# Performance work log

Measured on AMD Instinct MI355X. Metric: run time of the kernel, lower is better.

Reference implementation:

```python
import jax, jax.numpy as jnp
import numpy as np

L = 14  # max_relative_position
H = 12  # num_heads
HD = 64  # head_dim


def rel_pos_embed(N, table_v, table_h):
    # 2D relative-position embedding with a leading CLS token (index 0).
    n = N - 1
    s = int(n ** 0.5)  # grid side (14)
    r = jnp.arange(n)
    dv = r[None, :] // s - r[:, None] // s  # vertical distance
    dh = r[None, :] % s - r[:, None] % s   # horizontal distance
    iv = jnp.clip(dv, -L, L) + L + 1
    ih = jnp.clip(dh, -L, L) + L + 1
    iv = jnp.pad(iv, ((1, 0), (1, 0)))  # CLS row/col -> index 0
    ih = jnp.pad(ih, ((1, 0), (1, 0)))
    return table_v[iv] + table_h[ih]  # [N, N, HD]


def setup_inputs() -> dict:
    key = jax.random.key(0)
    ks = jax.random.split(key, 11)
    B, N, E = 64, 197, 768
    T = 2 * L + 2  # rel-pos table rows (30)
    std = 0.02
    return {
        "x": jax.random.normal(ks[0], (B, N, E), jnp.float32),
        "wq": jax.random.normal(ks[1], (E, H * HD), jnp.float32) * std,
        "wk": jax.random.normal(ks[2], (E, H * HD), jnp.float32) * std,
        "wv": jax.random.normal(ks[3], (E, H * HD), jnp.float32) * std,
        "wproj": jax.random.normal(ks[4], (H * HD, E), jnp.float32) * std,
        "bproj": jnp.zeros((E,), jnp.float32),
        "rk_v": jax.random.normal(ks[5], (T, HD), jnp.float32) * std,
        "rk_h": jax.random.normal(ks[6], (T, HD), jnp.float32) * std,
        "rv_v": jax.random.normal(ks[7], (T, HD), jnp.float32) * std,
        "rv_h": jax.random.normal(ks[8], (T, HD), jnp.float32) * std,
    }


def reference(x, wq, wk, wv, wproj, bproj, rk_v, rk_h, rv_v, rv_h):
    B, N, E = x.shape
    scale = HD ** -0.5
    q = (x @ wq).reshape(B, N, H, HD).transpose(0, 2, 1, 3)  # [B,H,N,HD]
    k = (x @ wk).reshape(B, N, H, HD).transpose(0, 2, 1, 3)
    v = (x @ wv).reshape(B, N, H, HD).transpose(0, 2, 1, 3)

    attn = jnp.einsum('bhid,bhjd->bhij', q, k) * scale
    rpk = rel_pos_embed(N, rk_v, rk_h)  # [N,N,HD]
    attn = attn + jnp.einsum('bhid,ijd->bhij', q, rpk) * scale
    attn = jax.nn.softmax(attn, axis=-1)

    out = jnp.einsum('bhij,bhjd->bhid', attn, v)
    rpv = rel_pos_embed(N, rv_v, rv_h)
    out = out + jnp.einsum('bhij,ijd->bhid', attn, rpv)

    out = out.transpose(0, 2, 1, 3).reshape(B, N, H * HD)
    return out @ wproj + bproj
```

## Files before the change

### kernel.cpp

```cpp
#include <hip/hip_runtime.h>
#include <math.h>

typedef _Float16 f16;
typedef __attribute__((ext_vector_type(8))) _Float16 f16x8;
typedef __attribute__((ext_vector_type(4))) _Float16 f16x4;
typedef __attribute__((ext_vector_type(4))) float f32x4;

#define NH 12
#define HDIM 64
#define NTOK 197
#define EDIM 768
#define NB 64
#define MROWS (NB*NTOK)

__device__ __forceinline__ void wfence() {
    asm volatile("s_waitcnt lgkmcnt(0)" ::: "memory");
    __builtin_amdgcn_sched_barrier(0);
    __builtin_amdgcn_wave_barrier();
}

__device__ __forceinline__ unsigned div14(unsigned n) { return (n * 4682u) >> 16; }

__device__ __forceinline__ void gload16(const f16* g, f16* lds_base) {
    __builtin_amdgcn_global_load_lds(
        (const __attribute__((address_space(1))) void*)g,
        (__attribute__((address_space(3))) void*)lds_base, 16, 0, 0);
}

__global__ __launch_bounds__(256) void prep_all(
    const float* __restrict__ x,
    const float* __restrict__ wq, const float* __restrict__ wk,
    const float* __restrict__ wv, const float* __restrict__ wp,
    const float* __restrict__ rkv, const float* __restrict__ rkh,
    f16* __restrict__ xh, f16* __restrict__ wqkvT, f16* __restrict__ wpT,
    f16* __restrict__ gA, f16* __restrict__ gt_buf)
{
    __shared__ float T[64][65];
    const int bid = blockIdx.x;
    if (bid < 4728) {
        int idx = bid * 256 + threadIdx.x;
        const float4* s = (const float4*)x + (size_t)idx * 2;
        float4 a = s[0], b = s[1];
        f16x8 h;
        h[0]=(f16)a.x; h[1]=(f16)a.y; h[2]=(f16)a.z; h[3]=(f16)a.w;
        h[4]=(f16)b.x; h[5]=(f16)b.y; h[6]=(f16)b.z; h[7]=(f16)b.w;
        *(f16x8*)(xh + (size_t)idx * 8) = h;
    } else if (bid < 5304) {
        int b2 = bid - 4728;
        int m = b2 / 144, rem = b2 - m*144;
        const float* src = (m==0)?wq:(m==1)?wk:(m==2)?wv:wp;
        int k0 = (rem / 12) * 64, n0 = (rem % 12) * 64;
        int cidx = threadIdx.x & 63, r4 = threadIdx.x >> 6;
#pragma unroll
        for (int rr = 0; rr < 16; ++rr) {
            int kl = rr*4 + r4;
            T[kl][cidx] = src[(size_t)(k0+kl)*EDIM + n0 + cidx];
        }
        __syncthreads();
        f16* dst = (m < 3) ? (wqkvT + (size_t)m*EDIM*EDIM) : wpT;
#pragma unroll
        for (int rr = 0; rr < 16; ++rr) {
            int nl = rr*4 + r4;
            dst[(size_t)(n0+nl)*EDIM + k0 + cidx] = (f16)T[cidx][nl];
        }
    } else {
        int t = (bid - 5304) * 256 + threadIdx.x;
        const int stride = 32 * 256;
        for (int i = t; i < 272*128; i += stride) {
            int row = i >> 7, cs = i & 127;
            int c = cs ^ ((row & 7) << 3);
            f16 v = (f16)0.f;
            if (c < 64) {
                if (row >= 208 && row < 238)      v = (f16)rkv[(row-208)*64 + c];
                else if (row >= 240 && row < 270) v = (f16)rkh[(row-240)*64 + c];
            } else if (c < 96 && row < 208) {
                int g = c - 64;
                if (row == 0) { if (g == 14 || g == 30) v = (f16)1.f; }
                else if (row <= 196) {
                    int rm = row - 1;
                    int gv = (int)div14((unsigned)rm), gh = rm - gv*14;
                    if (g == gv || g == 16 + gh) v = (f16)1.f;
                }
            }
            gA[i] = v;
        }
        for (int i = t; i < 32*256; i += stride) {
            int g = i >> 8, cs = i & 255;
            int j = cs ^ ((g & 7) << 3);
            f16 v = (f16)0.f;
            if (j >= 1 && j <= 196) {
                int jm = j - 1;
                int gv = (int)div14((unsigned)jm), gh = jm - gv*14;
                if ((g < 14 && gv == g) || (g >= 16 && g < 30 && gh == g - 16))
                    v = (f16)1.f;
            }
            gt_buf[i] = v;
        }
    }
}

__global__ __launch_bounds__(512, 2) void gemm256(
    const f16* __restrict__ A, const f16* __restrict__ Bt,
    f16* __restrict__ q_o, f16* __restrict__ k_o, f16* __restrict__ v_o,
    float* __restrict__ p_o, const float* __restrict__ bias, int mode, int nxb)
{
    __shared__ f16 lds[4*16384];

    const int tid = threadIdx.x;
    const int l = tid & 63, w = tid >> 6;
    const int lr = l & 15, lq = l >> 4;
    const int wr = w >> 2, wc = w & 3;

    const int nwg = gridDim.x, orig = blockIdx.x;
    const int xcd = orig & 7, qc = nwg >> 3, rc = nwg & 7;
    const int wgid = (xcd < rc ? xcd*(qc+1) : rc*(qc+1) + (xcd-rc)*qc) + (orig >> 3);
    const int mband = wgid / nxb, nband = wgid - mband*nxb;
    const int m0 = mband << 8, n0 = nband << 8;

    const int scol = (((tid & 7) ^ ((tid >> 3) & 7)) << 3);
    const f16* aG[4]; const f16* bG[4];
#pragma unroll
    for (int p = 0; p < 4; ++p) {
        int rt = p*64 + (tid >> 3);
        int ra = m0 + rt; if (ra >= MROWS) ra = MROWS - 1;
        aG[p] = A  + (size_t)ra * EDIM + scol;
        bG[p] = Bt + (size_t)(n0 + rt) * EDIM + scol;
    }
    const int lbase = w * 512;

    f32x4 acc[8][4];
#pragma unroll
    for (int mt = 0; mt < 8; ++mt)
#pragma unroll
        for (int nt = 0; nt < 4; ++nt) {
            acc[mt][nt][0]=0.f; acc[mt][nt][1]=0.f;
            acc[mt][nt][2]=0.f; acc[mt][nt][3]=0.f;
        }

#pragma unroll
    for (int p = 0; p < 4; ++p) {
        gload16(aG[p], &lds[p*4096 + lbase]);
        gload16(bG[p], &lds[32768 + p*4096 + lbase]);
    }
    asm volatile("s_waitcnt vmcnt(0)" ::: "memory");
    __builtin_amdgcn_sched_barrier(0);
    __builtin_amdgcn_s_barrier();

    const int swz = (lr & 7) << 3;
    int cur = 0;
    for (int kt = 0; kt < 12; ++kt) {
        if (kt < 11) {
            const int ko = (kt + 1) * 64;
            const int nb = (cur ^ 1) * 16384;
#pragma unroll
            for (int p = 0; p < 4; ++p) {
                gload16(aG[p] + ko, &lds[nb + p*4096 + lbase]);
                gload16(bG[p] + ko, &lds[32768 + nb + p*4096 + lbase]);
            }
        }
        __builtin_amdgcn_sched_barrier(0);
        const f16* Ab = &lds[cur * 16384];
        const f16* Bb = &lds[32768 + cur * 16384];
#pragma unroll
        for (int ks = 0; ks < 2; ++ks) {
            const int kb = (ks*32 + lq*8) ^ swz;
            f16x8 bf[4];
#pragma unroll
            for (int nt = 0; nt < 4; ++nt)
                bf[nt] = *(const f16x8*)&Bb[(wc*64 + nt*16 + lr)*64 + kb];
#pragma unroll
            for (int mt = 0; mt < 8; ++mt) {
                f16x8 af = *(const f16x8*)&Ab[(wr*128 + mt*16 + lr)*64 + kb];
#pragma unroll
                for (int nt = 0; nt < 4; ++nt)
                    acc[mt][nt] = __builtin_amdgcn_mfma_f32_16x16x32_f16(
                        af, bf[nt], acc[mt][nt], 0, 0, 0);
            }
        }
        asm volatile("s_waitcnt vmcnt(0)" ::: "memory");
        __builtin_amdgcn_sched_barrier(0);
        __builtin_amdgcn_s_barrier();
        cur ^= 1;
    }

    if (mode == 0) {
        const int mat   = n0 / EDIM;
        const int hbase = ((n0 % EDIM) >> 6) + wc;
        f16* dst = (mat == 0) ? q_o : (mat == 1) ? k_o : v_o;
        f16* scr = &lds[w * 2304];
#pragma unroll
        for (int mt2 = 0; mt2 < 4; ++mt2) {
#pragma unroll
            for (int mtp = 0; mtp < 2; ++mtp) {
                const int mt = mt2*2 + mtp;
#pragma unroll
                for (int nt = 0; nt < 4; ++nt)
#pragma unroll
                    for (int rg = 0; rg < 4; ++rg)
                        scr[(mtp*16 + lq*4 + rg)*72 + nt*16 + lr] = (f16)acc[mt][nt][rg];
            }
            wfence();
#pragma unroll
            for (int i = 0; i < 4; ++i) {
                int row = (l >> 3) + i*8;
                f16x8 v = *(const f16x8*)&scr[row*72 + (l & 7)*8];
                int R = m0 + wr*128 + mt2*32 + row;
                if (R < MROWS) {
                    int bb = R / NTOK, nn = R - bb*NTOK;
                    *(f16x8*)&dst[((size_t)(bb*NH + hbase)*NTOK + nn)*HDIM + (l & 7)*8] = v;
                }
            }
            wfence();
        }
    } else {
#pragma unroll
        for (int mt = 0; mt < 8; ++mt)
#pragma unroll
            for (int rg = 0; rg < 4; ++rg) {
                int R = m0 + wr*128 + mt*16 + lq*4 + rg;
                if (R < MROWS) {
                    float* base = p_o + (size_t)R * EDIM + n0 + wc*64;
#pragma unroll
                    for (int nt = 0; nt < 4; ++nt) {
                        int c = nt*16 + lr;
                        base[c] = acc[mt][nt][rg] + bias[n0 + wc*64 + c];
                    }
                }
            }
    }
}

#define SKE 128
#define SVT 320
#define SGT 256
#define SWS 72
#define ATHR 832

__global__ __launch_bounds__(ATHR, 1) void attn_mfma(
    const f16* __restrict__ q_ws, const f16* __restrict__ k_ws,
    const f16* __restrict__ v_ws,
    const float* __restrict__ rvv, const float* __restrict__ rvh,
    const f16* __restrict__ gA, const f16* __restrict__ gt_buf,
    f16* __restrict__ o_ws)
{
    __shared__ f16 Kle[272*SKE];
    __shared__ f16 Vt[64*SVT];
    __shared__ f16 Gt[32*SGT];
    __shared__ f16 WSh[13*16*SWS];

    const int tid = threadIdx.x;
    const int w = tid >> 6, l = tid & 63;
    const int lr = l & 15, lq = l >> 4;
    const int bh = blockIdx.x;
    const int b = bh / NH, h = bh - b * NH;
    const f16* Qp = q_ws + (size_t)bh * NTOK * HDIM;
    const f16* Kp = k_ws + (size_t)bh * NTOK * HDIM;
    const f16* Vp = v_ws + (size_t)bh * NTOK * HDIM;
    f16* wsh = &WSh[w * 16 * SWS];

    for (int idx = tid; idx < 272*16; idx += ATHR) {
        int row = idx >> 4, cs8 = (idx & 15) << 3;
        f16x8 v;
        if (row < NTOK && cs8 < 64) {
            int c8 = cs8 ^ ((row & 7) << 3);
            v = *(const f16x8*)(Kp + row*64 + c8);
        } else {
            v = *(const f16x8*)(gA + row*SKE + cs8);
        }
        *(f16x8*)&Kle[row*SKE + cs8] = v;
    }
    for (int idx = tid; idx < 32*32; idx += ATHR) {
        int off = idx * 8;
        *(f16x8*)&Gt[off] = *(const f16x8*)(gt_buf + off);
    }
    for (int idx = tid; idx < 8*SVT; idx += ATHR) {
        int dlow = idx & 7, k = idx >> 3;
        int kx = k ^ (dlow << 3);
        bool isV = (k < NTOK), isA = (k >= 208 && k < 238), isB = (k >= 238 && k < 268);
#pragma unroll
        for (int e = 0; e < 8; ++e) {
            int d = (e << 3) + dlow;
            f16 val = (f16)0.f;
            if (isV)      val = Vp[k*64 + d];
            else if (isA) val = (f16)rvv[(k-208)*64 + d];
            else if (isB) val = (f16)rvh[(k-238)*64 + d];
            Vt[d*SVT + kx] = val;
        }
    }
    __syncthreads();

    const int src0 = ((l >> 4) & 1) * 32 + lr;
    const int src1 = src0 + 16;

    {
        const int tt = w;
        const int i0 = tt * 16;
        const int iq = i0 + lr;
        const int iqc = (iq > 196) ? 196 : iq;
        const f16* qsrc = Qp + iqc*64 + lq*8;
        f16x8 qf0 = *(const f16x8*)qsrc;
        f16x8 qf1 = *(const f16x8*)(qsrc + 32);

        const int sw = (lr & 7) << 3;

        __builtin_amdgcn_s_setprio(1);
        f32x4 pacc[4];
#pragma unroll
        for (int ct = 0; ct < 4; ++ct) {
            f32x4 a; a[0]=0.f; a[1]=0.f; a[2]=0.f; a[3]=0.f;
            const int krow = (13+ct)*16 + lr;
            f16x8 kf0 = *(f16x8*)&Kle[krow*SKE + ((lq*8) ^ sw)];
            f16x8 kf1 = *(f16x8*)&Kle[krow*SKE + ((32 + lq*8) ^ sw)];
            a = __builtin_amdgcn_mfma_f32_16x16x32_f16(kf0, qf0, a, 0, 0, 0);
            a = __builtin_amdgcn_mfma_f32_16x16x32_f16(kf1, qf1, a, 0, 0, 0);
            pacc[ct] = a;
        }
        __builtin_amdgcn_s_setprio(0);
#pragma unroll
        for (int ct = 0; ct < 4; ++ct)
#pragma unroll
            for (int rg = 0; rg < 4; ++rg)
                wsh[lr*SWS + ct*16 + lq*4 + rg] = (f16)pacc[ct][rg];
        wfence();

        int id_ = 0, ih_ = 0;
        const bool qcls = (iq == 0);
        if (iq > 0) { unsigned v = div14((unsigned)(iq-1)); id_ = (int)v; ih_ = (iq-1) - (int)v*14; }
        f16x8 qcf;
#pragma unroll
        for (int e = 0; e < 8; ++e) {
            int g = lq*8 + e;
            int toff;
            if (g < 14)       toff = qcls ? 0 : (g - id_ + 15);
            else if (g == 14) toff = 0;
            else if (g == 15) toff = 63;
            else if (g < 30)  toff = qcls ? 32 : (32 + (g-16) - ih_ + 15);
            else if (g == 30) toff = 32;
            else              toff = 63;
            qcf[e] = wsh[lr*SWS + toff];
        }

        f32x4 acc[13];
        __builtin_amdgcn_s_setprio(1);
#pragma unroll
        for (int ct = 0; ct < 13; ++ct) {
            f32x4 a; a[0]=0.f; a[1]=0.f; a[2]=0.f; a[3]=0.f;
            const int krow = ct*16 + lr;
            f16x8 kf0 = *(f16x8*)&Kle[krow*SKE + ((lq*8) ^ sw)];
            f16x8 kf1 = *(f16x8*)&Kle[krow*SKE + ((32 + lq*8) ^ sw)];
            f16x8 gf  = *(f16x8*)&Kle[krow*SKE + ((64 + lq*8) ^ sw)];
            a = __builtin_amdgcn_mfma_f32_16x16x32_f16(kf0, qf0, a, 0, 0, 0);
            a = __builtin_amdgcn_mfma_f32_16x16x32_f16(kf1, qf1, a, 0, 0, 0);
            a = __builtin_amdgcn_mfma_f32_16x16x32_f16(gf,  qcf, a, 0, 0, 0);
            acc[ct] = a;
        }
        __builtin_amdgcn_s_setprio(0);

#pragma unroll
        for (int rg = 0; rg < 4; ++rg)
            if (lq*4 + rg > 4) acc[12][rg] = -1e30f;

        float m = -1e30f;
#pragma unroll
        for (int ct = 0; ct < 13; ++ct)
#pragma unroll
            for (int rg = 0; rg < 4; ++rg) m = fmaxf(m, acc[ct][rg]);
        m = fmaxf(m, __shfl_xor(m, 16));
        m = fmaxf(m, __shfl_xor(m, 32));
        const float C1 = 0.125f * 1.44269504088896f;
        const float nm = -m * C1;
        float ssum = 0.f;
#pragma unroll
        for (int ct = 0; ct < 13; ++ct)
#pragma unroll
            for (int rg = 0; rg < 4; ++rg) {
                float p = exp2f(fmaf(acc[ct][rg], C1, nm));
                acc[ct][rg] = p; ssum += p;
            }
        ssum += __shfl_xor(ssum, 16);
        ssum += __shfl_xor(ssum, 32);
        const float inv = 1.f / ssum;
        const float pn00 = acc[0][0] * inv;

        unsigned pk[13][2];
#pragma unroll
        for (int ct = 0; ct < 13; ++ct) {
            union { f16x4 hh; unsigned u[2]; } t;
            t.hh[0] = (f16)(acc[ct][0] * inv);
            t.hh[1] = (f16)(acc[ct][1] * inv);
            t.hh[2] = (f16)(acc[ct][2] * inv);
            t.hh[3] = (f16)(acc[ct][3] * inv);
            pk[ct][0] = t.u[0]; pk[ct][1] = t.u[1];
        }

        f16x8 pa[7];
#pragma unroll
        for (int kc = 0; kc < 7; ++kc) {
            const int ctA = 2*kc;
            const int ctB = (kc == 6) ? 12 : 2*kc + 1;
            unsigned A0 = (unsigned)__shfl((int)pk[ctA][0], src0);
            unsigned A1 = (unsigned)__shfl((int)pk[ctA][1], src0);
            unsigned A2 = (unsigned)__shfl((int)pk[ctA][0], src1);
            unsigned A3 = (unsigned)__shfl((int)pk[ctA][1], src1);
            unsigned B0 = (unsigned)__shfl((int)pk[ctB][0], src0);
            unsigned B1 = (unsigned)__shfl((int)pk[ctB][1], src0);
            unsigned B2 = (unsigned)__shfl((int)pk[ctB][0], src1);
            unsigned B3 = (unsigned)__shfl((int)pk[ctB][1], src1);
            bool hiHalf = (lq >= 2);
            union { unsigned u[4]; f16x8 v; } f;
            f.u[0] = hiHalf ? B0 : A0;
            f.u[1] = hiHalf ? B1 : A1;
            f.u[2] = hiHalf ? B2 : A2;
            f.u[3] = hiHalf ? B3 : A3;
            if (kc == 6 && hiHalf) { f.u[0]=0; f.u[1]=0; f.u[2]=0; f.u[3]=0; }
            pa[kc] = f.v;
        }

        f32x4 gacc[2];
#pragma unroll
        for (int ct = 0; ct < 2; ++ct) { gacc[ct][0]=0.f; gacc[ct][1]=0.f; gacc[ct][2]=0.f; gacc[ct][3]=0.f; }
        __builtin_amdgcn_s_setprio(1);
#pragma unroll
        for (int kc = 0; kc < 7; ++kc) {
#pragma unroll
            for (int ct = 0; ct < 2; ++ct) {
                f16x8 gf = *(f16x8*)&Gt[(ct*16 + lr)*SGT + ((kc*32 + lq*8) ^ sw)];
                gacc[ct] = __builtin_amdgcn_mfma_f32_16x16x32_f16(pa[kc], gf, gacc[ct], 0, 0, 0);
            }
        }
        __builtin_amdgcn_s_setprio(0);

#pragma unroll
        for (int z = 0; z < 2; ++z) {
            int zi = z*64 + l;
            int zr = zi >> 3, zc = (zi & 7) << 3;
            f16x8 zz;
#pragma unroll
            for (int e = 0; e < 8; ++e) zz[e] = (f16)0.f;
            *(f16x8*)&wsh[zr*SWS + zc] = zz;
        }
        wfence();
#pragma unroll
        for (int rg = 0; rg < 4; ++rg) {
            int il = lq*4 + rg;
            int is_ = i0 + il;
            if (lr < 14 && is_ > 0) {
                unsigned v = div14((unsigned)(is_-1));
                int id2 = (int)v, ih2 = (is_-1) - (int)v*14;
                wsh[il*SWS + (lr - id2 + 15)]      = (f16)gacc[0][rg];
                wsh[il*SWS + 30 + (lr - ih2 + 15)] = (f16)gacc[1][rg];
            }
        }
        if (lq == 0 && !(i0 == 0 && lr == 0)) {
            wsh[lr*SWS + 0]  = (f16)pn00;
            wsh[lr*SWS + 30] = (f16)pn00;
        }
        if (i0 == 0) {
            float sv = (lq == 0) ? gacc[0][0] : 0.f;
            float sh = (lq == 0) ? gacc[1][0] : 0.f;
            sv += __shfl_xor(sv, 1); sv += __shfl_xor(sv, 2);
            sv += __shfl_xor(sv, 4); sv += __shfl_xor(sv, 8);
            sh += __shfl_xor(sh, 1); sh += __shfl_xor(sh, 2);
            sh += __shfl_xor(sh, 4); sh += __shfl_xor(sh, 8);
            if (l == 0) {
                wsh[0]  = (f16)(sv + pn00);
                wsh[30] = (f16)(sh + pn00);
            }
        }
        wfence();

        f16x8 sfr[2];
#pragma unroll
        for (int kc2 = 0; kc2 < 2; ++kc2)
            sfr[kc2] = *(f16x8*)&wsh[lr*SWS + kc2*32 + lq*8];

        f32x4 oacc[4];
#pragma unroll
        for (int ct = 0; ct < 4; ++ct) { oacc[ct][0]=0.f; oacc[ct][1]=0.f; oacc[ct][2]=0.f; oacc[ct][3]=0.f; }
        __builtin_amdgcn_s_setprio(1);
#pragma unroll
        for (int kc = 0; kc < 7; ++kc) {
#pragma unroll
            for (int ct = 0; ct < 4; ++ct) {
                f16x8 vf = *(f16x8*)&Vt[(ct*16 + lr)*SVT + ((kc*32 + lq*8) ^ sw)];
                oacc[ct] = __builtin_amdgcn_mfma_f32_16x16x32_f16(pa[kc], vf, oacc[ct], 0, 0, 0);
            }
        }
#pragma unroll
        for (int kc2 = 0; kc2 < 2; ++kc2) {
#pragma unroll
            for (int ct = 0; ct < 4; ++ct) {
                f16x8 vf = *(f16x8*)&Vt[(ct*16 + lr)*SVT + ((208 + kc2*32 + lq*8) ^ sw)];
                oacc[ct] = __builtin_amdgcn_mfma_f32_16x16x32_f16(sfr[kc2], vf, oacc[ct], 0, 0, 0);
            }
        }
        __builtin_amdgcn_s_setprio(0);

#pragma unroll
        for (int ct = 0; ct < 4; ++ct)
#pragma unroll
            for (int rg = 0; rg < 4; ++rg) {
                int io = i0 + lq*4 + rg;
                if (io < NTOK) {
                    int d = ct*16 + lr;
                    o_ws[((size_t)(b * NTOK + io) * NH + h) * HDIM + d] = (f16)oacc[ct][rg];
                }
            }
    }
}

extern "C" void kernel_launch(void* const* d_in, const int* in_sizes, int n_in,
                              void* d_out, int out_size, void* d_ws, size_t ws_size,
                              hipStream_t stream)
{
    const float* x     = (const float*)d_in[0];
    const float* wq    = (const float*)d_in[1];
    const float* wk    = (const float*)d_in[2];
    const float* wv    = (const float*)d_in[3];
    const float* wproj = (const float*)d_in[4];
    const float* bproj = (const float*)d_in[5];
    const float* rkv   = (const float*)d_in[6];
    const float* rkh   = (const float*)d_in[7];
    const float* rvv   = (const float*)d_in[8];
    const float* rvh   = (const float*)d_in[9];

    f16* ws = (f16*)d_ws;
    const size_t sz = (size_t)MROWS * EDIM;
    f16* xh    = ws;
    f16* qh    = xh + sz;
    f16* kh    = qh + sz;
    f16* vh    = kh + sz;
    f16* oh    = vh + sz;
    f16* wqkvT = oh + sz;
    f16* wpT   = wqkvT + (size_t)3*EDIM*EDIM;
    f16* gA    = wpT   + (size_t)EDIM*EDIM;
    f16* gtb   = gA    + 272*128;

    prep_all<<<5336, 256, 0, stream>>>(x, wq, wk, wv, wproj, rkv, rkh,
                                       xh, wqkvT, wpT, gA, gtb);
    gemm256 <<<50*9, 512, 0, stream>>>(xh, wqkvT, qh, kh, vh,
                                       nullptr, nullptr, 0, 9);
    attn_mfma<<<NB * NH, ATHR, 0, stream>>>(qh, kh, vh,
                                            rvv, rvh, gA, gtb, oh);
    gemm256 <<<50*3, 512, 0, stream>>>(oh, wpT, nullptr, nullptr, nullptr,
                                       (float*)d_out, bproj, 1, 3);
}
```

Measured before the change: 148.1 us.

## Fuse x fp32-to-fp16 conversion into QKV GEMM and async-load attention K/G tiles

After: 150.5 us. Within noise of the previous version (+1.6%).

```diff
diff --git a/kernel.cpp b/kernel.cpp
--- a/kernel.cpp
+++ b/kernel.cpp
@@ -28,26 +28,16 @@
 }
 
 __global__ __launch_bounds__(256) void prep_all(
-    const float* __restrict__ x,
     const float* __restrict__ wq, const float* __restrict__ wk,
     const float* __restrict__ wv, const float* __restrict__ wp,
     const float* __restrict__ rkv, const float* __restrict__ rkh,
-    f16* __restrict__ xh, f16* __restrict__ wqkvT, f16* __restrict__ wpT,
+    f16* __restrict__ wqkvT, f16* __restrict__ wpT,
     f16* __restrict__ gA, f16* __restrict__ gt_buf)
 {
     __shared__ float T[64][65];
     const int bid = blockIdx.x;
-    if (bid < 4728) {
-        int idx = bid * 256 + threadIdx.x;
-        const float4* s = (const float4*)x + (size_t)idx * 2;
-        float4 a = s[0], b = s[1];
-        f16x8 h;
-        h[0]=(f16)a.x; h[1]=(f16)a.y; h[2]=(f16)a.z; h[3]=(f16)a.w;
-        h[4]=(f16)b.x; h[5]=(f16)b.y; h[6]=(f16)b.z; h[7]=(f16)b.w;
-        *(f16x8*)(xh + (size_t)idx * 8) = h;
-    } else if (bid < 5304) {
-        int b2 = bid - 4728;
-        int m = b2 / 144, rem = b2 - m*144;
+    if (bid < 576) {
+        int m = bid / 144, rem = bid - m*144;
         const float* src = (m==0)?wq:(m==1)?wk:(m==2)?wv:wp;
         int k0 = (rem / 12) * 64, n0 = (rem % 12) * 64;
         int cidx = threadIdx.x & 63, r4 = threadIdx.x >> 6;
@@ -64,7 +54,7 @@
             dst[(size_t)(n0+nl)*EDIM + k0 + cidx] = (f16)T[cidx][nl];
         }
     } else {
-        int t = (bid - 5304) * 256 + threadIdx.x;
+        int t = (bid - 576) * 256 + threadIdx.x;
         const int stride = 32 * 256;
         for (int i = t; i < 272*128; i += stride) {
             int row = i >> 7, cs = i & 127;
@@ -99,8 +89,9 @@
     }
 }
 
-__global__ __launch_bounds__(512, 2) void gemm256(
-    const f16* __restrict__ A, const f16* __restrict__ Bt,
+template<bool AF32>
+__global__ __launch_bounds__(512, 2) void gemm256T(
+    const void* __restrict__ Ain, const f16* __restrict__ Bt,
     f16* __restrict__ q_o, f16* __restrict__ k_o, f16* __restrict__ v_o,
     float* __restrict__ p_o, const float* __restrict__ bias, int mode, int nxb)
 {
@@ -118,15 +109,19 @@
     const int m0 = mband << 8, n0 = nband << 8;
 
     const int scol = (((tid & 7) ^ ((tid >> 3) & 7)) << 3);
-    const f16* aG[4]; const f16* bG[4];
+    const f16* bG[4];
+    const f16* aGh[4];
+    const float* aGf[4];
 #pragma unroll
     for (int p = 0; p < 4; ++p) {
         int rt = p*64 + (tid >> 3);
         int ra = m0 + rt; if (ra >= MROWS) ra = MROWS - 1;
-        aG[p] = A  + (size_t)ra * EDIM + scol;
+        if (AF32) aGf[p] = (const float*)Ain + (size_t)ra * EDIM + ((tid & 7) << 3);
+        else      aGh[p] = (const f16*)Ain + (size_t)ra * EDIM + scol;
         bG[p] = Bt + (size_t)(n0 + rt) * EDIM + scol;
     }
     const int lbase = w * 512;
+    const int dstA = (tid >> 3)*64 + scol;
 
     f32x4 acc[8][4];
 #pragma unroll
@@ -137,14 +132,32 @@
             acc[mt][nt][2]=0.f; acc[mt][nt][3]=0.f;
         }
 
-#pragma unroll
-    for (int p = 0; p < 4; ++p) {
-        gload16(aG[p], &lds[p*4096 + lbase]);
+    float4 ar0[4], ar1[4];
+#pragma unroll
+    for (int p = 0; p < 4; ++p)
         gload16(bG[p], &lds[32768 + p*4096 + lbase]);
-    }
-    asm volatile("s_waitcnt vmcnt(0)" ::: "memory");
-    __builtin_amdgcn_sched_barrier(0);
-    __builtin_amdgcn_s_barrier();
+    if (AF32) {
+#pragma unroll
+        for (int p = 0; p < 4; ++p) {
+            ar0[p] = *(const float4*)(aGf[p]);
+            ar1[p] = *(const float4*)(aGf[p] + 4);
+        }
+#pragma unroll
+        for (int p = 0; p < 4; ++p) {
+            f16x8 h;
+            h[0]=(f16)ar0[p].x; h[1]=(f16)ar0[p].y; h[2]=(f16)ar0[p].z; h[3]=(f16)ar0[p].w;
+            h[4]=(f16)ar1[p].x; h[5]=(f16)ar1[p].y; h[6]=(f16)ar1[p].z; h[7]=(f16)ar1[p].w;
+            *(f16x8*)&lds[p*4096 + dstA] = h;
+        }
+        __syncthreads();
+    } else {
+#pragma unroll
+        for (int p = 0; p < 4; ++p)
+            gload16(aGh[p], &lds[p*4096 + lbase]);
+        asm volatile("s_waitcnt vmcnt(0)" ::: "memory");
+        __builtin_amdgcn_sched_barrier(0);
+        __builtin_amdgcn_s_barrier();
+    }
 
     const int swz = (lr & 7) << 3;
     int cur = 0;
@@ -153,9 +166,18 @@
             const int ko = (kt + 1) * 64;
             const int nb = (cur ^ 1) * 16384;
 #pragma unroll
-            for (int p = 0; p < 4; ++p) {
-                gload16(aG[p] + ko, &lds[nb + p*4096 + lbase]);
+            for (int p = 0; p < 4; ++p)
                 gload16(bG[p] + ko, &lds[32768 + nb + p*4096 + lbase]);
+            if (AF32) {
+#pragma unroll
+                for (int p = 0; p < 4; ++p) {
+                    ar0[p] = *(const float4*)(aGf[p] + ko);
+                    ar1[p] = *(const float4*)(aGf[p] + ko + 4);
+                }
+            } else {
+#pragma unroll
+                for (int p = 0; p < 4; ++p)
+                    gload16(aGh[p] + ko, &lds[nb + p*4096 + lbase]);
             }
         }
         __builtin_amdgcn_sched_barrier(0);
@@ -177,9 +199,23 @@
                         af, bf[nt], acc[mt][nt], 0, 0, 0);
             }
         }
-        asm volatile("s_waitcnt vmcnt(0)" ::: "memory");
-        __builtin_amdgcn_sched_barrier(0);
-        __builtin_amdgcn_s_barrier();
+        if (AF32) {
+            if (kt < 11) {
+                const int nb = (cur ^ 1) * 16384;
+#pragma unroll
+                for (int p = 0; p < 4; ++p) {
+                    f16x8 h;
+                    h[0]=(f16)ar0[p].x; h[1]=(f16)ar0[p].y; h[2]=(f16)ar0[p].z; h[3]=(f16)ar0[p].w;
+                    h[4]=(f16)ar1[p].x; h[5]=(f16)ar1[p].y; h[6]=(f16)ar1[p].z; h[7]=(f16)ar1[p].w;
+                    *(f16x8*)&lds[nb + p*4096 + dstA] = h;
+                }
+            }
+            __syncthreads();
+        } else {
+            asm volatile("s_waitcnt vmcnt(0)" ::: "memory");
+            __builtin_amdgcn_sched_barrier(0);
+            __builtin_amdgcn_s_barrier();
+        }
         cur ^= 1;
     }
 
@@ -258,51 +294,58 @@
     const f16* Vp = v_ws + (size_t)bh * NTOK * HDIM;
     f16* wsh = &WSh[w * 16 * SWS];
 
-    for (int idx = tid; idx < 272*16; idx += ATHR) {
-        int row = idx >> 4, cs8 = (idx & 15) << 3;
-        f16x8 v;
-        if (row < NTOK && cs8 < 64) {
-            int c8 = cs8 ^ ((row & 7) << 3);
-            v = *(const f16x8*)(Kp + row*64 + c8);
+    for (int c = w; c < 84; c += 13) {
+        f16* ldsb;
+        const f16* gsrc;
+        if (c < 68) {
+            int idx = c*64 + l;
+            int row = idx >> 4, cs8 = (idx & 15) << 3;
+            ldsb = &Kle[c * 512];
+            gsrc = (row < NTOK && cs8 < 64)
+                 ? (Kp + row*64 + (cs8 ^ ((row & 7) << 3)))
+                 : (gA + row*SKE + cs8);
         } else {
-            v = *(const f16x8*)(gA + row*SKE + cs8);
-        }
-        *(f16x8*)&Kle[row*SKE + cs8] = v;
-    }
-    for (int idx = tid; idx < 32*32; idx += ATHR) {
-        int off = idx * 8;
-        *(f16x8*)&Gt[off] = *(const f16x8*)(gt_buf + off);
-    }
-    for (int idx = tid; idx < 8*SVT; idx += ATHR) {
-        int dlow = idx & 7, k = idx >> 3;
-        int kx = k ^ (dlow << 3);
-        bool isV = (k < NTOK), isA = (k >= 208 && k < 238), isB = (k >= 238 && k < 268);
-#pragma unroll
-        for (int e = 0; e < 8; ++e) {
-            int d = (e << 3) + dlow;
-            f16 val = (f16)0.f;
-            if (isV)      val = Vp[k*64 + d];
-            else if (isA) val = (f16)rvv[(k-208)*64 + d];
-            else if (isB) val = (f16)rvh[(k-238)*64 + d];
-            Vt[d*SVT + kx] = val;
-        }
-    }
+            int c2 = c - 68;
+            ldsb = &Gt[c2 * 512];
+            gsrc = gt_buf + c2*512 + l*8;
+        }
+        gload16(gsrc, ldsb);
+    }
+
+    f16x8 vbuf[4];
+#pragma unroll
+    for (int it = 0; it < 4; ++it) {
+        int idx = tid + it*ATHR;
+        if (idx < 8*SVT) {
+            int dlow = idx & 7, k = idx >> 3;
+            bool isV = (k < NTOK), isA = (k >= 208 && k < 238), isB = (k >= 238 && k < 268);
+#pragma unroll
+            for (int e = 0; e < 8; ++e) {
+                int d = (e << 3) + dlow;
+                f16 val = (f16)0.f;
+                if (isV)      val = Vp[k*64 + d];
+                else if (isA) val = (f16)rvv[(k-208)*64 + d];
+                else if (isB) val = (f16)rvh[(k-238)*64 + d];
+                vbuf[it][e] = val;
+            }
+        }
+    }
+
+    const int tt = w;
+    const int i0 = tt * 16;
+    const int iq = i0 + lr;
+    const int iqc = (iq > 196) ? 196 : iq;
+    const f16* qsrc = Qp + iqc*64 + lq*8;
+    f16x8 qf0 = *(const f16x8*)qsrc;
+    f16x8 qf1 = *(const f16x8*)(qsrc + 32);
+
     __syncthreads();
 
     const int src0 = ((l >> 4) & 1) * 32 + lr;
     const int src1 = src0 + 16;
+    const int sw = (lr & 7) << 3;
 
     {
-        const int tt = w;
-        const int i0 = tt * 16;
-        const int iq = i0 + lr;
-        const int iqc = (iq > 196) ? 196 : iq;
-        const f16* qsrc = Qp + iqc*64 + lq*8;
-        f16x8 qf0 = *(const f16x8*)qsrc;
-        f16x8 qf1 = *(const f16x8*)(qsrc + 32);
-
-        const int sw = (lr & 7) << 3;
-
         __builtin_amdgcn_s_setprio(1);
         f32x4 pacc[4];
 #pragma unroll
@@ -469,6 +512,19 @@
         }
         wfence();
 
+#pragma unroll
+        for (int it = 0; it < 4; ++it) {
+            int idx = tid + it*ATHR;
+            if (idx < 8*SVT) {
+                int dlow = idx & 7, k = idx >> 3;
+                int kx = k ^ (dlow << 3);
+#pragma unroll
+                for (int e = 0; e < 8; ++e)
+                    Vt[((e << 3) + dlow)*SVT + kx] = vbuf[it][e];
+            }
+        }
+        __syncthreads();
+
         f16x8 sfr[2];
 #pragma unroll
         for (int kc2 = 0; kc2 < 2; ++kc2)
@@ -526,8 +582,7 @@
 
     f16* ws = (f16*)d_ws;
     const size_t sz = (size_t)MROWS * EDIM;
-    f16* xh    = ws;
-    f16* qh    = xh + sz;
+    f16* qh    = ws;
     f16* kh    = qh + sz;
     f16* vh    = kh + sz;
     f16* oh    = vh + sz;
@@ -536,12 +591,12 @@
     f16* gA    = wpT   + (size_t)EDIM*EDIM;
     f16* gtb   = gA    + 272*128;
 
-    prep_all<<<5336, 256, 0, stream>>>(x, wq, wk, wv, wproj, rkv, rkh,
-                                       xh, wqkvT, wpT, gA, gtb);
-    gemm256 <<<50*9, 512, 0, stream>>>(xh, wqkvT, qh, kh, vh,
-                                       nullptr, nullptr, 0, 9);
+    prep_all<<<608, 256, 0, stream>>>(wq, wk, wv, wproj, rkv, rkh,
+                                      wqkvT, wpT, gA, gtb);
+    gemm256T<true><<<50*9, 512, 0, stream>>>(x, wqkvT, qh, kh, vh,
+                                             nullptr, nullptr, 0, 9);
     attn_mfma<<<NB * NH, ATHR, 0, stream>>>(qh, kh, vh,
                                             rvv, rvh, gA, gtb, oh);
-    gemm256 <<<50*3, 512, 0, stream>>>(oh, wpT, nullptr, nullptr, nullptr,
-                                       (float*)d_out, bproj, 1, 3);
+    gemm256T<false><<<50*3, 512, 0, stream>>>(oh, wpT, nullptr, nullptr, nullptr,
+                                              (float*)d_out, bproj, 1, 3);
 }
```

## Load K and G tiles via global_load_lds and defer V transpose past score phase

Applied to the files above, without the earlier changes.

Measured after the change: 144.2 us, median of 3. 1.03x faster.

```diff
diff --git a/kernel.cpp b/kernel.cpp
--- a/kernel.cpp
+++ b/kernel.cpp
@@ -258,51 +258,58 @@
     const f16* Vp = v_ws + (size_t)bh * NTOK * HDIM;
     f16* wsh = &WSh[w * 16 * SWS];
 
-    for (int idx = tid; idx < 272*16; idx += ATHR) {
-        int row = idx >> 4, cs8 = (idx & 15) << 3;
-        f16x8 v;
-        if (row < NTOK && cs8 < 64) {
-            int c8 = cs8 ^ ((row & 7) << 3);
-            v = *(const f16x8*)(Kp + row*64 + c8);
+    for (int c = w; c < 84; c += 13) {
+        f16* ldsb;
+        const f16* gsrc;
+        if (c < 68) {
+            int idx = c*64 + l;
+            int row = idx >> 4, cs8 = (idx & 15) << 3;
+            ldsb = &Kle[c * 512];
+            gsrc = (row < NTOK && cs8 < 64)
+                 ? (Kp + row*64 + (cs8 ^ ((row & 7) << 3)))
+                 : (gA + row*SKE + cs8);
         } else {
-            v = *(const f16x8*)(gA + row*SKE + cs8);
-        }
-        *(f16x8*)&Kle[row*SKE + cs8] = v;
-    }
-    for (int idx = tid; idx < 32*32; idx += ATHR) {
-        int off = idx * 8;
-        *(f16x8*)&Gt[off] = *(const f16x8*)(gt_buf + off);
-    }
-    for (int idx = tid; idx < 8*SVT; idx += ATHR) {
-        int dlow = idx & 7, k = idx >> 3;
-        int kx = k ^ (dlow << 3);
-        bool isV = (k < NTOK), isA = (k >= 208 && k < 238), isB = (k >= 238 && k < 268);
-#pragma unroll
-        for (int e = 0; e < 8; ++e) {
-            int d = (e << 3) + dlow;
-            f16 val = (f16)0.f;
-            if (isV)      val = Vp[k*64 + d];
-            else if (isA) val = (f16)rvv[(k-208)*64 + d];
-            else if (isB) val = (f16)rvh[(k-238)*64 + d];
-            Vt[d*SVT + kx] = val;
-        }
-    }
+            int c2 = c - 68;
+            ldsb = &Gt[c2 * 512];
+            gsrc = gt_buf + c2*512 + l*8;
+        }
+        gload16(gsrc, ldsb);
+    }
+
+    f16x8 vbuf[4];
+#pragma unroll
+    for (int it = 0; it < 4; ++it) {
+        int idx = tid + it*ATHR;
+        if (idx < 8*SVT) {
+            int dlow = idx & 7, k = idx >> 3;
+            bool isV = (k < NTOK), isA = (k >= 208 && k < 238), isB = (k >= 238 && k < 268);
+#pragma unroll
+            for (int e = 0; e < 8; ++e) {
+                int d = (e << 3) + dlow;
+                f16 val = (f16)0.f;
+                if (isV)      val = Vp[k*64 + d];
+                else if (isA) val = (f16)rvv[(k-208)*64 + d];
+                else if (isB) val = (f16)rvh[(k-238)*64 + d];
+                vbuf[it][e] = val;
+            }
+        }
+    }
+
+    const int tt = w;
+    const int i0 = tt * 16;
+    const int iq = i0 + lr;
+    const int iqc = (iq > 196) ? 196 : iq;
+    const f16* qsrc = Qp + iqc*64 + lq*8;
+    f16x8 qf0 = *(const f16x8*)qsrc;
+    f16x8 qf1 = *(const f16x8*)(qsrc + 32);
+
     __syncthreads();
 
     const int src0 = ((l >> 4) & 1) * 32 + lr;
     const int src1 = src0 + 16;
+    const int sw = (lr & 7) << 3;
 
     {
-        const int tt = w;
-        const int i0 = tt * 16;
-        const int iq = i0 + lr;
-        const int iqc = (iq > 196) ? 196 : iq;
-        const f16* qsrc = Qp + iqc*64 + lq*8;
-        f16x8 qf0 = *(const f16x8*)qsrc;
-        f16x8 qf1 = *(const f16x8*)(qsrc + 32);
-
-        const int sw = (lr & 7) << 3;
-
         __builtin_amdgcn_s_setprio(1);
         f32x4 pacc[4];
 #pragma unroll
@@ -469,6 +476,19 @@
         }
         wfence();
 
+#pragma unroll
+        for (int it = 0; it < 4; ++it) {
+            int idx = tid + it*ATHR;
+            if (idx < 8*SVT) {
+                int dlow = idx & 7, k = idx >> 3;
+                int kx = k ^ (dlow << 3);
+#pragma unroll
+                for (int e = 0; e < 8; ++e)
+                    Vt[((e << 3) + dlow)*SVT + kx] = vbuf[it][e];
+            }
+        }
+        __syncthreads();
+
         f16x8 sfr[2];
 #pragma unroll
         for (int kc2 = 0; kc2 < 2; ++kc2)
```
